# Performance work log

Measured on AMD Instinct MI355X. Metric: run time of the kernel, lower is better.

Reference implementation:

```python
import jax, jax.numpy as jnp
import numpy as np

N = 100000      # nodes
D = 64          # input feature dim
L0, L1 = 64, 32 # layer sizes
EP = 400000     # positive edges
EN = 400000     # negative edges
LAMB = 1.0


def _scatter_mean(feats, rows, num_nodes):
    # mean of feats grouped by destination node `rows`; empty nodes -> 0
    s = jax.ops.segment_sum(feats, rows, num_segments=num_nodes)
    c = jax.ops.segment_sum(jnp.ones((rows.shape[0],), feats.dtype), rows, num_segments=num_nodes)
    return s / jnp.maximum(c, 1.0)[:, None]


def _base_layer(x, edges, W, b):
    row, col = edges[0], edges[1]
    agg = _scatter_mean(x[col], row, x.shape[0])          # [N, D]
    return jnp.tanh(jnp.concatenate([agg, x], axis=1) @ W + b)


def _deep_layer(x1, x2, pos_edges, neg_edges, W, b):
    agg1 = _scatter_mean(x1[pos_edges[1]], pos_edges[0], x1.shape[0])
    agg2 = _scatter_mean(x2[neg_edges[1]], neg_edges[0], x2.shape[0])
    return jnp.tanh(jnp.concatenate([agg1, agg2, x1], axis=1) @ W + b)


def _xavier(key, shape):
    fan_in, fan_out = shape[0], shape[1]
    lim = np.sqrt(6.0 / (fan_in + fan_out)).astype(np.float32)
    return jax.random.uniform(key, shape, jnp.float32, -lim, lim)


def setup_inputs() -> dict:
    key = jax.random.key(0)
    ks = jax.random.split(key, 12)
    X = jax.random.normal(ks[0], (N, D), jnp.float32)
    W_pos0 = _xavier(ks[1], (2 * D, L0)); b_pos0 = jnp.zeros((L0,), jnp.float32)
    W_neg0 = _xavier(ks[2], (2 * D, L0)); b_neg0 = jnp.zeros((L0,), jnp.float32)
    W_pos1 = _xavier(ks[3], (3 * L0, L1)); b_pos1 = jnp.zeros((L1,), jnp.float32)
    W_neg1 = _xavier(ks[4], (3 * L0, L1)); b_neg1 = jnp.zeros((L1,), jnp.float32)
    W_reg = _xavier(ks[5], (4 * L1, 2))
    positive_edges = jax.random.randint(ks[6], (2, EP), 0, N)
    negative_edges = jax.random.randint(ks[7], (2, EN), 0, N)
    target = jax.random.randint(ks[8], (EP + EN,), 0, 2)
    pos_samples = jax.random.randint(ks[9], (EP,), 0, N)
    neg_samples = jax.random.randint(ks[10], (EN,), 0, N)
    return {"X": X, "W_pos0": W_pos0, "b_pos0": b_pos0, "W_neg0": W_neg0,
            "b_neg0": b_neg0, "W_pos1": W_pos1, "b_pos1": b_pos1,
            "W_neg1": W_neg1, "b_neg1": b_neg1, "W_reg": W_reg,
            "positive_edges": positive_edges, "negative_edges": negative_edges,
            "target": target, "pos_samples": pos_samples, "neg_samples": neg_samples}


def _triplet_loss(z, edges, samples):
    zi = z[edges[0]]
    zj = z[edges[1]]
    zk = z[samples]
    norm_ij = jnp.sum((zi - zj) ** 2, axis=1)
    norm_ik = jnp.sum((zj - zk) ** 2, axis=1)
    return jnp.mean(jnp.maximum(norm_ij - norm_ik, 0.0)), zi, zj


def reference(X, W_pos0, b_pos0, W_neg0, b_neg0, W_pos1, b_pos1,
              W_neg1, b_neg1, W_reg, positive_edges, negative_edges,
              target, pos_samples, neg_samples):
    h_pos = _base_layer(X, positive_edges, W_pos0, b_pos0)
    h_neg = _base_layer(X, negative_edges, W_neg0, b_neg0)
    h_pos2 = _deep_layer(h_pos, h_neg, positive_edges, negative_edges, W_pos1, b_pos1)
    h_neg2 = _deep_layer(h_neg, h_pos, positive_edges, negative_edges, W_neg1, b_neg1)
    z = jnp.concatenate([h_pos2, h_neg2], axis=1)  # [N, 2*L1]

    loss_pos, pzi, pzj = _triplet_loss(z, positive_edges, pos_samples)
    loss_neg, nzi, nzj = _triplet_loss(z, negative_edges, neg_samples)

    feats = jnp.concatenate([
        jnp.concatenate([pzi, pzj], axis=1),
        jnp.concatenate([nzi, nzj], axis=1)], axis=0)       # [EP+EN, 4*L1]
    logp = jax.nn.log_softmax(feats @ W_reg, axis=1)
    regress = -jnp.mean(jnp.take_along_axis(logp, target[:, None], axis=1))
    loss = regress + LAMB * (loss_pos + loss_neg)
    return (loss, z)
```

## Files before the change

### kernel.cpp

```cpp
#include <hip/hip_runtime.h>
#include <cstdint>

#define N_NODES 100000
#define EP_N 400000
#define EN_N 400000
#define NODE_BLOCKS ((N_NODES + 63) / 64)
#define SCHUNK 512
#define SBLK ((N_NODES + SCHUNK - 1) / SCHUNK)

#define BSTR 264
#define DSTR 392

#define XB_BLKS ((((N_NODES + 1) * 16) + 255) / 256)
#define WP_BLKS 112
#define CNT_BLKS (((EP_N + EN_N) + 255) / 256)

#define ACC_OFF 0
#define I_CNTP 16
#define I_CNTN (I_CNTP + N_NODES)
#define I_CURP (I_CNTN + N_NODES)
#define I_CURN (I_CURP + N_NODES)
#define I_OFFP (I_CURN + N_NODES)
#define I_OFFN (I_OFFP + N_NODES + 1)
#define I_CSRP (((I_OFFN + N_NODES + 1) + 3) & ~3)
#define CSR_SZ (EP_N + 4 * N_NODES)
#define I_CSRN (I_CSRP + CSR_SZ)
#define I_PART (I_CSRN + CSR_SZ)
#define F_XB (((I_PART + 2 * SBLK) + 15) & ~15)
#define F_HB (F_XB + 32 * (N_NODES + 1))
#define F_PN (F_HB + 64 * (N_NODES + 1))
#define F_ZQ (F_PN + 8 * N_NODES)
#define F_WT (((F_ZQ + 16 * N_NODES) + 15) & ~15)

typedef __attribute__((ext_vector_type(8))) short sh8;
typedef __attribute__((ext_vector_type(4))) float f32x4;

__device__ inline float bf2f(unsigned short u) {
    return __uint_as_float((unsigned)u << 16);
}
__device__ inline unsigned short f2bf(float v) {
    unsigned u = __float_as_uint(v);
    return (unsigned short)((u + 0x7FFFu + ((u >> 16) & 1u)) >> 16);
}
__device__ inline float lo_bf(unsigned u) { return __uint_as_float(u << 16); }
__device__ inline float hi_bf(unsigned u) { return __uint_as_float(u & 0xFFFF0000u); }

__global__ void prep_kernel(const float* __restrict__ X, unsigned short* __restrict__ xb,
                            const float* __restrict__ W0p, const float* __restrict__ W0n,
                            const float* __restrict__ W1p, const float* __restrict__ W1n,
                            unsigned short* __restrict__ wt,
                            const int* __restrict__ pe, const int* __restrict__ ne,
                            int* cp, int* cn) {
    int b = blockIdx.x;
    if (b < XB_BLKS) {
        int i = b * 256 + threadIdx.x;
        if (i < (N_NODES + 1) * 16) {
            ushort4 o = {0, 0, 0, 0};
            if (i < N_NODES * 16) {
                float4 v = ((const float4*)X)[i];
                o.x = f2bf(v.x); o.y = f2bf(v.y); o.z = f2bf(v.z); o.w = f2bf(v.w);
            }
            ((ushort4*)xb)[i] = o;
        }
    } else if (b < XB_BLKS + WP_BLKS) {
        int i = (b - XB_BLKS) * 256 + threadIdx.x;
        if (i < 8192) {
            int n = i >> 7, k = i & 127;
            wt[i] = f2bf(W0p[k * 64 + n]);
        } else if (i < 16384) {
            int j = i - 8192; int n = j >> 7, k = j & 127;
            wt[i] = f2bf(W0n[k * 64 + n]);
        } else if (i < 22528) {
            int j = i - 16384; int n = j / 192, k = j - n * 192;
            wt[i] = f2bf(W1p[k * 32 + n]);
        } else if (i < 28672) {
            int j = i - 22528; int n = j / 192, k = j - n * 192;
            wt[i] = f2bf(W1n[k * 32 + n]);
        }
    } else {
        int i = (b - XB_BLKS - WP_BLKS) * 256 + threadIdx.x;
        if (i < EP_N) {
            atomicAdd(&cp[pe[i]], 1);
        } else if (i < EP_N + EN_N) {
            atomicAdd(&cn[ne[i - EP_N]], 1);
        }
    }
}

__global__ __launch_bounds__(512) void scan_p1(const int* __restrict__ cntP,
                                               const int* __restrict__ cntN,
                                               int* part) {
    int l = blockIdx.x < SBLK ? 0 : 1;
    int blk = blockIdx.x - l * SBLK;
    const int* cnt = l == 0 ? cntP : cntN;
    int idx = blk * SCHUNK + threadIdx.x;
    int v = idx < N_NODES ? (cnt[idx] + 3) & ~3 : 0;
    __shared__ int tmp[512];
    tmp[threadIdx.x] = v;
    __syncthreads();
    for (int d = 256; d > 0; d >>= 1) {
        if (threadIdx.x < d) tmp[threadIdx.x] += tmp[threadIdx.x + d];
        __syncthreads();
    }
    if (threadIdx.x == 0) part[l * SBLK + blk] = tmp[0];
}

__global__ __launch_bounds__(512) void scan_p2(int* part) {
    int t = threadIdx.x;
    int l = t >> 8, idx = t & 255;
    int v = idx < SBLK ? part[l * SBLK + idx] : 0;
    __shared__ int tmp[512];
    int sb = l << 8;
    tmp[sb + idx] = v;
    __syncthreads();
    for (int d = 1; d < 256; d <<= 1) {
        int x = (idx >= d) ? tmp[sb + idx - d] : 0;
        __syncthreads();
        tmp[sb + idx] += x;
        __syncthreads();
    }
    if (idx < SBLK) part[l * SBLK + idx] = tmp[sb + idx] - v;
}

__global__ __launch_bounds__(512) void scan_p3(const int* __restrict__ cntP,
                                               const int* __restrict__ cntN,
                                               const int* __restrict__ part,
                                               int* offP, int* offN,
                                               int* csrP, int* csrN) {
    int l = blockIdx.x < SBLK ? 0 : 1;
    int blk = blockIdx.x - l * SBLK;
    const int* cnt = l == 0 ? cntP : cntN;
    int* off = l == 0 ? offP : offN;
    int* csr = l == 0 ? csrP : csrN;
    int base = part[l * SBLK + blk];
    int t = threadIdx.x;
    int gidx = blk * SCHUNK + t;
    int c = gidx < N_NODES ? cnt[gidx] : 0;
    int cpad = (c + 3) & ~3;
    __shared__ int tmp[512];
    tmp[t] = cpad;
    __syncthreads();
    for (int d = 1; d < 512; d <<= 1) {
        int x = (t >= d) ? tmp[t - d] : 0;
        __syncthreads();
        tmp[t] += x;
        __syncthreads();
    }
    int incl = tmp[t];
    if (gidx < N_NODES) {
        int o = base + incl - cpad;
        off[gidx] = o;
        for (int p = c; p < cpad; ++p) csr[o + p] = N_NODES;
    }
    if (gidx == N_NODES - 1) off[N_NODES] = base + incl;
}

__global__ void fill_kernel(const int* __restrict__ pe, const int* __restrict__ ne,
                            const int* __restrict__ offP, const int* __restrict__ offN,
                            int* curP, int* curN, int* csrP, int* csrN) {
    int e = blockIdx.x * 256 + threadIdx.x;
    if (e < EP_N) {
        int row = pe[e], col = pe[EP_N + e];
        int slot = atomicAdd(&curP[row], 1);
        csrP[offP[row] + slot] = col;
    } else if (e < EP_N + EN_N) {
        int e2 = e - EP_N;
        int row = ne[e2], col = ne[EN_N + e2];
        int slot = atomicAdd(&curN[row], 1);
        csrN[offN[row] + slot] = col;
    }
}

__device__ inline float gather_mean_b(const unsigned short* __restrict__ src,
                                      const int* __restrict__ csr,
                                      int st, int en, int cnt, int lane) {
    float s0 = 0.f, s1 = 0.f, s2 = 0.f, s3 = 0.f;
    for (int p = st; p < en; p += 4) {
        int4 c4 = *(const int4*)(csr + p);
        s0 += bf2f(src[c4.x * 64 + lane]);
        s1 += bf2f(src[c4.y * 64 + lane]);
        s2 += bf2f(src[c4.z * 64 + lane]);
        s3 += bf2f(src[c4.w * 64 + lane]);
    }
    return ((s0 + s1) + (s2 + s3)) / fmaxf((float)cnt, 1.0f);
}

__device__ inline void gather2(const unsigned* __restrict__ hb32,
                               const int* __restrict__ csr,
                               int st, int en, int cnt, int lane,
                               float& mp, float& mn) {
    float p0 = 0.f, p1 = 0.f, p2 = 0.f, p3 = 0.f;
    float n0 = 0.f, n1 = 0.f, n2 = 0.f, n3 = 0.f;
    for (int p = st; p < en; p += 4) {
        int4 c4 = *(const int4*)(csr + p);
        unsigned v0 = hb32[c4.x * 64 + lane];
        unsigned v1 = hb32[c4.y * 64 + lane];
        unsigned v2 = hb32[c4.z * 64 + lane];
        unsigned v3 = hb32[c4.w * 64 + lane];
        p0 += lo_bf(v0); n0 += hi_bf(v0);
        p1 += lo_bf(v1); n1 += hi_bf(v1);
        p2 += lo_bf(v2); n2 += hi_bf(v2);
        p3 += lo_bf(v3); n3 += hi_bf(v3);
    }
    float d = 1.0f / fmaxf((float)cnt, 1.0f);
    mp = ((p0 + p1) + (p2 + p3)) * d;
    mn = ((n0 + n1) + (n2 + n3)) * d;
}

__global__ __launch_bounds__(512) void base_both(
    const unsigned short* __restrict__ xb,
    const int* __restrict__ offP, const int* __restrict__ csrP,
    const int* __restrict__ offN, const int* __restrict__ csrN,
    const int* __restrict__ cntP, const int* __restrict__ cntN,
    const unsigned short* __restrict__ wt0,
    const float* __restrict__ bp0, const float* __restrict__ bn0,
    unsigned short* __restrict__ hboth) {
    __shared__ unsigned short lds[64 * BSTR];
    int tid = threadIdx.x, lane = tid & 63, w = tid >> 6;
    int base = blockIdx.x * 64;
    if (blockIdx.x == 0 && tid < 64) ((unsigned*)hboth)[N_NODES * 64 + tid] = 0u;
    for (int r = w * 8; r < w * 8 + 8; ++r) {
        int node = base + r;
        float gP = 0.f, gN = 0.f;
        unsigned short sx = 0;
        if (node < N_NODES) {
            gP = gather_mean_b(xb, csrP, offP[node], offP[node + 1], cntP[node], lane);
            gN = gather_mean_b(xb, csrN, offN[node], offN[node + 1], cntN[node], lane);
            sx = xb[node * 64 + lane];
        }
        unsigned short* rp = &lds[r * BSTR];
        rp[lane] = f2bf(gP);
        rp[64 + lane] = sx;
        rp[128 + lane] = f2bf(gN);
        rp[192 + lane] = sx;
    }
    __syncthreads();
    int wu = __builtin_amdgcn_readfirstlane(w);
    int mt = wu >> 1, half = wu & 1;
    int l15 = lane & 15, kq = lane >> 4;
    const unsigned short* wbase = wt0 + half * 8192;
    f32x4 acc[4];
#pragma unroll
    for (int nt = 0; nt < 4; ++nt) acc[nt] = (f32x4){0.f, 0.f, 0.f, 0.f};
    const unsigned short* arow = &lds[(mt * 16 + l15) * BSTR + half * 128 + kq * 8];
#pragma unroll
    for (int ks = 0; ks < 4; ++ks) {
        sh8 a = *(const sh8*)(arow + ks * 32);
#pragma unroll
        for (int nt = 0; nt < 4; ++nt) {
            sh8 bf = *(const sh8*)(wbase + (nt * 16 + l15) * 128 + ks * 32 + kq * 8);
            acc[nt] = __builtin_amdgcn_mfma_f32_16x16x32_bf16(a, bf, acc[nt], 0, 0, 0);
        }
    }
    __syncthreads();
    float* ht = (float*)lds;
    const float* bias = half ? bn0 : bp0;
#pragma unroll
    for (int nt = 0; nt < 4; ++nt) {
        int col = nt * 16 + l15;
        float bb = bias[col];
#pragma unroll
        for (int r = 0; r < 4; ++r) {
            int row = mt * 16 + kq * 4 + r;
            ht[row * 130 + half * 64 + col] = tanhf(acc[nt][r] + bb);
        }
    }
    __syncthreads();
    unsigned* hb32 = (unsigned*)hboth;
    for (int i = tid; i < 64 * 64; i += 512) {
        int rr = i >> 6, c = i & 63;
        int node = base + rr;
        if (node < N_NODES) {
            unsigned lo = f2bf(ht[rr * 130 + c]);
            unsigned hi = f2bf(ht[rr * 130 + 64 + c]);
            hb32[node * 64 + c] = lo | (hi << 16);
        }
    }
}

__global__ __launch_bounds__(512) void deep_both(
    const unsigned short* __restrict__ hb,
    const int* __restrict__ offP, const int* __restrict__ csrP,
    const int* __restrict__ offN, const int* __restrict__ csrN,
    const int* __restrict__ cntP, const int* __restrict__ cntN,
    const unsigned short* __restrict__ wt1,
    const float* __restrict__ bp1, const float* __restrict__ bn1,
    const float* __restrict__ Wreg, float* __restrict__ z,
    unsigned char* __restrict__ zq, float* __restrict__ pn) {
    __shared__ unsigned short lds[64 * DSTR];
    int tid = threadIdx.x, lane = tid & 63, w = tid >> 6;
    int base = blockIdx.x * 64;
    const unsigned* hb32 = (const unsigned*)hb;
    for (int r = w * 8; r < w * 8 + 8; ++r) {
        int node = base + r;
        float gPp = 0.f, gPn = 0.f, gNp = 0.f, gNn = 0.f, sp = 0.f, sn = 0.f;
        if (node < N_NODES) {
            gather2(hb32, csrP, offP[node], offP[node + 1], cntP[node], lane, gPp, gPn);
            gather2(hb32, csrN, offN[node], offN[node + 1], cntN[node], lane, gNp, gNn);
            unsigned self = hb32[node * 64 + lane];
            sp = lo_bf(self);
            sn = hi_bf(self);
        }
        unsigned short* rp = &lds[r * DSTR];
        rp[lane] = f2bf(gPp);
        rp[64 + lane] = f2bf(gNn);
        rp[128 + lane] = f2bf(sp);
        rp[192 + lane] = f2bf(gPn);
        rp[256 + lane] = f2bf(gNp);
        rp[320 + lane] = f2bf(sn);
    }
    __syncthreads();
    int wu = __builtin_amdgcn_readfirstlane(w);
    int mt = wu >> 1, half = wu & 1;
    int l15 = lane & 15, kq = lane >> 4;
    const unsigned short* wbase = wt1 + half * 6144;
    f32x4 acc[2];
    acc[0] = (f32x4){0.f, 0.f, 0.f, 0.f};
    acc[1] = (f32x4){0.f, 0.f, 0.f, 0.f};
    const unsigned short* arow = &lds[(mt * 16 + l15) * DSTR + half * 192 + kq * 8];
#pragma unroll
    for (int ks = 0; ks < 6; ++ks) {
        sh8 a = *(const sh8*)(arow + ks * 32);
#pragma unroll
        for (int nt = 0; nt < 2; ++nt) {
            sh8 bf = *(const sh8*)(wbase + (nt * 16 + l15) * 192 + ks * 32 + kq * 8);
            acc[nt] = __builtin_amdgcn_mfma_f32_16x16x32_bf16(a, bf, acc[nt], 0, 0, 0);
        }
    }
    __syncthreads();
    float* ot = (float*)lds;
    const float* bias = half ? bn1 : bp1;
#pragma unroll
    for (int nt = 0; nt < 2; ++nt) {
        int col = nt * 16 + l15;
        float bb = bias[col];
#pragma unroll
        for (int r = 0; r < 4; ++r) {
            int row = mt * 16 + kq * 4 + r;
            ot[row * 65 + half * 32 + col] = tanhf(acc[nt][r] + bb);
        }
    }
    __syncthreads();
    for (int r = w * 8; r < w * 8 + 8; ++r) {
        int node = base + r;
        if (node >= N_NODES) break;
        float v = ot[r * 65 + lane];
        z[node * 64 + lane] = v;
        int pq = __builtin_amdgcn_cvt_pk_fp8_f32(v, v, 0, false);
        zq[node * 64 + lane] = (unsigned char)(pq & 0xFF);
        float vq = __builtin_amdgcn_cvt_f32_fp8(pq, 0);
        float u0 = vq * Wreg[lane * 2 + 0];
        float u1 = vq * Wreg[lane * 2 + 1];
        float v0 = vq * Wreg[128 + lane * 2 + 0];
        float v1 = vq * Wreg[128 + lane * 2 + 1];
        float s = vq * vq;
#pragma unroll
        for (int off = 32; off; off >>= 1) {
            u0 += __shfl_xor(u0, off);
            u1 += __shfl_xor(u1, off);
            v0 += __shfl_xor(v0, off);
            v1 += __shfl_xor(v1, off);
            s += __shfl_xor(s, off);
        }
        if (lane == 0) {
            float4 st = {u0, u1, v0, v1};
            *(float4*)(pn + node * 8) = st;
            pn[node * 8 + 4] = s;
        }
    }
}

__global__ __launch_bounds__(256) void loss4_kernel(
    const unsigned char* __restrict__ zq, const float* __restrict__ pn,
    const int* __restrict__ pe, const int* __restrict__ ne,
    const int* __restrict__ ps, const int* __restrict__ ns,
    const int* __restrict__ tgt, float* acc) {
    int tid = threadIdx.x;
    int lane = tid & 63;
    int g = lane >> 4, sub = lane & 15;
    int wid = (blockIdx.x * 256 + tid) >> 6;
    int nw = (gridDim.x * 256) >> 6;
    float s_p = 0.f, s_n = 0.f, s_r = 0.f;
    const float q = 0.0625f;
    for (int eb = wid * 8; eb < EP_N + EN_N; eb += nw * 8) {
        int eA = eb + g, eB = eb + 4 + g;
        bool vA = eA < EP_N + EN_N, vB = eB < EP_N + EN_N;
        bool pA = eA < EP_N, pB = eB < EP_N;
        int iA = 0, jA = 0, kA = 0, tA = 0, iB = 0, jB = 0, kB = 0, tB = 0;
        if (vA) {
            if (pA) { iA = pe[eA]; jA = pe[EP_N + eA]; kA = ps[eA]; }
            else { int e2 = eA - EP_N; iA = ne[e2]; jA = ne[EN_N + e2]; kA = ns[e2]; }
            tA = tgt[eA];
        }
        if (vB) {
            if (pB) { iB = pe[eB]; jB = pe[EP_N + eB]; kB = ps[eB]; }
            else { int e2 = eB - EP_N; iB = ne[e2]; jB = ne[EN_N + e2]; kB = ns[e2]; }
            tB = tgt[eB];
        }
        unsigned ziA = *(const unsigned*)(zq + ((long long)iA << 6) + (sub << 2));
        unsigned zjA = *(const unsigned*)(zq + ((long long)jA << 6) + (sub << 2));
        unsigned zkA = *(const unsigned*)(zq + ((long long)kA << 6) + (sub << 2));
        unsigned ziB = *(const unsigned*)(zq + ((long long)iB << 6) + (sub << 2));
        unsigned zjB = *(const unsigned*)(zq + ((long long)jB << 6) + (sub << 2));
        unsigned zkB = *(const unsigned*)(zq + ((long long)kB << 6) + (sub << 2));
        const float* pniA = pn + ((long long)iA << 3);
        const float* pnjA = pn + ((long long)jA << 3);
        float u0A = pniA[0], u1A = pniA[1], siA = pniA[4];
        float v0A = pnjA[2], v1A = pnjA[3], sjA = pnjA[4];
        float skA = pn[((long long)kA << 3) + 4];
        const float* pniB = pn + ((long long)iB << 3);
        const float* pnjB = pn + ((long long)jB << 3);
        float u0B = pniB[0], u1B = pniB[1], siB = pniB[4];
        float v0B = pnjB[2], v1B = pnjB[3], sjB = pnjB[4];
        float skB = pn[((long long)kB << 3) + 4];
        float d1A, d2A, d1B, d2B;
        {
            float i0 = __builtin_amdgcn_cvt_f32_fp8(ziA, 0), i1 = __builtin_amdgcn_cvt_f32_fp8(ziA, 1);
            float i2 = __builtin_amdgcn_cvt_f32_fp8(ziA, 2), i3 = __builtin_amdgcn_cvt_f32_fp8(ziA, 3);
            float j0 = __builtin_amdgcn_cvt_f32_fp8(zjA, 0), j1 = __builtin_amdgcn_cvt_f32_fp8(zjA, 1);
            float j2 = __builtin_amdgcn_cvt_f32_fp8(zjA, 2), j3 = __builtin_amdgcn_cvt_f32_fp8(zjA, 3);
            float k0 = __builtin_amdgcn_cvt_f32_fp8(zkA, 0), k1 = __builtin_amdgcn_cvt_f32_fp8(zkA, 1);
            float k2 = __builtin_amdgcn_cvt_f32_fp8(zkA, 2), k3 = __builtin_amdgcn_cvt_f32_fp8(zkA, 3);
            d1A = fmaf(i0, j0, fmaf(i1, j1, fmaf(i2, j2, i3 * j3)));
            d2A = fmaf(j0, k0, fmaf(j1, k1, fmaf(j2, k2, j3 * k3)));
        }
        {
            float i0 = __builtin_amdgcn_cvt_f32_fp8(ziB, 0), i1 = __builtin_amdgcn_cvt_f32_fp8(ziB, 1);
            float i2 = __builtin_amdgcn_cvt_f32_fp8(ziB, 2), i3 = __builtin_amdgcn_cvt_f32_fp8(ziB, 3);
            float j0 = __builtin_amdgcn_cvt_f32_fp8(zjB, 0), j1 = __builtin_amdgcn_cvt_f32_fp8(zjB, 1);
            float j2 = __builtin_amdgcn_cvt_f32_fp8(zjB, 2), j3 = __builtin_amdgcn_cvt_f32_fp8(zjB, 3);
            float k0 = __builtin_amdgcn_cvt_f32_fp8(zkB, 0), k1 = __builtin_amdgcn_cvt_f32_fp8(zkB, 1);
            float k2 = __builtin_amdgcn_cvt_f32_fp8(zkB, 2), k3 = __builtin_amdgcn_cvt_f32_fp8(zkB, 3);
            d1B = fmaf(i0, j0, fmaf(i1, j1, fmaf(i2, j2, i3 * j3)));
            d2B = fmaf(j0, k0, fmaf(j1, k1, fmaf(j2, k2, j3 * k3)));
        }
#pragma unroll
        for (int off = 1; off < 16; off <<= 1) {
            d1A += __shfl_xor(d1A, off);
            d2A += __shfl_xor(d2A, off);
            d1B += __shfl_xor(d1B, off);
            d2B += __shfl_xor(d2B, off);
        }
        if (vA) {
            float nij = siA + sjA - 2.f * d1A;
            float nik = sjA + skA - 2.f * d2A;
            float tri = fmaxf(nij - nik, 0.f);
            float l0 = u0A + v0A, l1 = u1A + v1A;
            float m = fmaxf(l0, l1);
            float lse = m + logf(expf(l0 - m) + expf(l1 - m));
            s_r += (lse - (tA ? l1 : l0)) * q;
            if (pA) s_p += tri * q; else s_n += tri * q;
        }
        if (vB) {
            float nij = siB + sjB - 2.f * d1B;
            float nik = sjB + skB - 2.f * d2B;
            float tri = fmaxf(nij - nik, 0.f);
            float l0 = u0B + v0B, l1 = u1B + v1B;
            float m = fmaxf(l0, l1);
            float lse = m + logf(expf(l0 - m) + expf(l1 - m));
            s_r += (lse - (tB ? l1 : l0)) * q;
            if (pB) s_p += tri * q; else s_n += tri * q;
        }
    }
#pragma unroll
    for (int off = 32; off; off >>= 1) {
        s_p += __shfl_xor(s_p, off);
        s_n += __shfl_xor(s_n, off);
        s_r += __shfl_xor(s_r, off);
    }
    __shared__ float red[3][4];
    int w = tid >> 6;
    if (lane == 0) {
        red[0][w] = s_p; red[1][w] = s_n; red[2][w] = s_r;
    }
    __syncthreads();
    if (tid == 0) {
        atomicAdd(&acc[0], red[0][0] + red[0][1] + red[0][2] + red[0][3]);
        atomicAdd(&acc[1], red[1][0] + red[1][1] + red[1][2] + red[1][3]);
        atomicAdd(&acc[2], red[2][0] + red[2][1] + red[2][2] + red[2][3]);
    }
}

__global__ void finalize_kernel(const float* __restrict__ acc, float* out) {
    out[0] = acc[2] / (float)(EP_N + EN_N) +
             1.0f * (acc[0] / (float)EP_N + acc[1] / (float)EN_N);
}

extern "C" void kernel_launch(void* const* d_in, const int* in_sizes, int n_in,
                              void* d_out, int out_size, void* d_ws, size_t ws_size,
                              hipStream_t stream) {
    const float* X = (const float*)d_in[0];
    const float* W_pos0 = (const float*)d_in[1];
    const float* b_pos0 = (const float*)d_in[2];
    const float* W_neg0 = (const float*)d_in[3];
    const float* b_neg0 = (const float*)d_in[4];
    const float* W_pos1 = (const float*)d_in[5];
    const float* b_pos1 = (const float*)d_in[6];
    const float* W_neg1 = (const float*)d_in[7];
    const float* b_neg1 = (const float*)d_in[8];
    const float* W_reg = (const float*)d_in[9];
    const int* pe = (const int*)d_in[10];
    const int* ne = (const int*)d_in[11];
    const int* target = (const int*)d_in[12];
    const int* ps = (const int*)d_in[13];
    const int* ns = (const int*)d_in[14];
    float* out = (float*)d_out;
    float* ws = (float*)d_ws;
    int* wsi = (int*)d_ws;

    float* acc = ws + ACC_OFF;
    int* cntP = wsi + I_CNTP;
    int* cntN = wsi + I_CNTN;
    int* curP = wsi + I_CURP;
    int* curN = wsi + I_CURN;
    int* offP = wsi + I_OFFP;
    int* offN = wsi + I_OFFN;
    int* csrP = wsi + I_CSRP;
    int* csrN = wsi + I_CSRN;
    int* part = wsi + I_PART;
    unsigned short* xb = (unsigned short*)(ws + F_XB);
    unsigned short* hboth = (unsigned short*)(ws + F_HB);
    float* pn = ws + F_PN;
    unsigned char* zq = (unsigned char*)(ws + F_ZQ);
    unsigned short* wt = (unsigned short*)(ws + F_WT);
    float* z = out + 1;

    hipMemsetAsync(ws, 0, (size_t)(16 + 4 * N_NODES) * sizeof(float), stream);

    prep_kernel<<<XB_BLKS + WP_BLKS + CNT_BLKS, 256, 0, stream>>>(
        X, xb, W_pos0, W_neg0, W_pos1, W_neg1, wt, pe, ne, cntP, cntN);
    scan_p1<<<2 * SBLK, 512, 0, stream>>>(cntP, cntN, part);
    scan_p2<<<1, 512, 0, stream>>>(part);
    scan_p3<<<2 * SBLK, 512, 0, stream>>>(cntP, cntN, part, offP, offN, csrP, csrN);
    fill_kernel<<<(EP_N + EN_N + 255) / 256, 256, 0, stream>>>(pe, ne, offP, offN,
                                                               curP, curN, csrP, csrN);

    base_both<<<NODE_BLOCKS, 512, 0, stream>>>(xb, offP, csrP, offN, csrN, cntP, cntN,
                                               wt, b_pos0, b_neg0, hboth);
    deep_both<<<NODE_BLOCKS, 512, 0, stream>>>(hboth, offP, csrP, offN, csrN, cntP, cntN,
                                               wt + 16384, b_pos1, b_neg1,
                                               W_reg, z, zq, pn);

    loss4_kernel<<<2048, 256, 0, stream>>>(zq, pn, pe, ne, ps, ns, target, acc);
    finalize_kernel<<<1, 1, 0, stream>>>(acc, out);
}
```

Before: 410.4 us.

## Interleave pos/neg CSR gathers and pack per-edge indices and node stats

The base and deep layers now walk the positive and negative neighbour lists in one interleaved loop, so twice as many independent gather loads are in flight per iteration. The prep kernel packs each edge's (i, j, sample, target) into an int4 array. The per-node stats are split into two float4 arrays (u0,u1,s) and (v0,v1,s), so the loss kernel does one vector load for the indices and one per node instead of many scalar loads. The cost is an extra pass that writes 12.8 MB of packed indices, plus higher register pressure in the gather loops.

```diff
diff --git a/kernel.cpp b/kernel.cpp
--- a/kernel.cpp
+++ b/kernel.cpp
@@ -14,6 +14,7 @@
 #define XB_BLKS ((((N_NODES + 1) * 16) + 255) / 256)
 #define WP_BLKS 112
 #define CNT_BLKS (((EP_N + EN_N) + 255) / 256)
+#define EI_BLKS CNT_BLKS
 
 #define ACC_OFF 0
 #define I_CNTP 16
@@ -26,10 +27,12 @@
 #define CSR_SZ (EP_N + 4 * N_NODES)
 #define I_CSRN (I_CSRP + CSR_SZ)
 #define I_PART (I_CSRN + CSR_SZ)
-#define F_XB (((I_PART + 2 * SBLK) + 15) & ~15)
+#define I_EIDX (((I_PART + 2 * SBLK) + 3) & ~3)
+#define F_XB (((I_EIDX + 4 * (EP_N + EN_N)) + 15) & ~15)
 #define F_HB (F_XB + 32 * (N_NODES + 1))
-#define F_PN (F_HB + 64 * (N_NODES + 1))
-#define F_ZQ (F_PN + 8 * N_NODES)
+#define F_PNU (F_HB + 64 * (N_NODES + 1))
+#define F_PNV (F_PNU + 4 * N_NODES)
+#define F_ZQ (F_PNV + 4 * N_NODES)
 #define F_WT (((F_ZQ + 16 * N_NODES) + 15) & ~15)
 
 typedef __attribute__((ext_vector_type(8))) short sh8;
@@ -50,7 +53,9 @@
                             const float* __restrict__ W1p, const float* __restrict__ W1n,
                             unsigned short* __restrict__ wt,
                             const int* __restrict__ pe, const int* __restrict__ ne,
-                            int* cp, int* cn) {
+                            const int* __restrict__ ps, const int* __restrict__ ns,
+                            const int* __restrict__ tgt,
+                            int* cp, int* cn, int4* __restrict__ eidx) {
     int b = blockIdx.x;
     if (b < XB_BLKS) {
         int i = b * 256 + threadIdx.x;
@@ -77,12 +82,22 @@
             int j = i - 22528; int n = j / 192, k = j - n * 192;
             wt[i] = f2bf(W1n[k * 32 + n]);
         }
-    } else {
+    } else if (b < XB_BLKS + WP_BLKS + CNT_BLKS) {
         int i = (b - XB_BLKS - WP_BLKS) * 256 + threadIdx.x;
         if (i < EP_N) {
             atomicAdd(&cp[pe[i]], 1);
         } else if (i < EP_N + EN_N) {
             atomicAdd(&cn[ne[i - EP_N]], 1);
+        }
+    } else {
+        int e = (b - XB_BLKS - WP_BLKS - CNT_BLKS) * 256 + threadIdx.x;
+        if (e < EP_N) {
+            int4 q = {pe[e], pe[EP_N + e], ps[e], tgt[e]};
+            eidx[e] = q;
+        } else if (e < EP_N + EN_N) {
+            int e2 = e - EP_N;
+            int4 q = {ne[e2], ne[EN_N + e2], ns[e2], tgt[e]};
+            eidx[e] = q;
         }
     }
 }
@@ -171,40 +186,100 @@
     }
 }
 
-__device__ inline float gather_mean_b(const unsigned short* __restrict__ src,
-                                      const int* __restrict__ csr,
-                                      int st, int en, int cnt, int lane) {
-    float s0 = 0.f, s1 = 0.f, s2 = 0.f, s3 = 0.f;
-    for (int p = st; p < en; p += 4) {
-        int4 c4 = *(const int4*)(csr + p);
-        s0 += bf2f(src[c4.x * 64 + lane]);
-        s1 += bf2f(src[c4.y * 64 + lane]);
-        s2 += bf2f(src[c4.z * 64 + lane]);
-        s3 += bf2f(src[c4.w * 64 + lane]);
-    }
-    return ((s0 + s1) + (s2 + s3)) / fmaxf((float)cnt, 1.0f);
-}
-
-__device__ inline void gather2(const unsigned* __restrict__ hb32,
-                               const int* __restrict__ csr,
-                               int st, int en, int cnt, int lane,
-                               float& mp, float& mn) {
-    float p0 = 0.f, p1 = 0.f, p2 = 0.f, p3 = 0.f;
-    float n0 = 0.f, n1 = 0.f, n2 = 0.f, n3 = 0.f;
-    for (int p = st; p < en; p += 4) {
-        int4 c4 = *(const int4*)(csr + p);
-        unsigned v0 = hb32[c4.x * 64 + lane];
-        unsigned v1 = hb32[c4.y * 64 + lane];
-        unsigned v2 = hb32[c4.z * 64 + lane];
-        unsigned v3 = hb32[c4.w * 64 + lane];
-        p0 += lo_bf(v0); n0 += hi_bf(v0);
-        p1 += lo_bf(v1); n1 += hi_bf(v1);
-        p2 += lo_bf(v2); n2 += hi_bf(v2);
-        p3 += lo_bf(v3); n3 += hi_bf(v3);
-    }
-    float d = 1.0f / fmaxf((float)cnt, 1.0f);
-    mp = ((p0 + p1) + (p2 + p3)) * d;
-    mn = ((n0 + n1) + (n2 + n3)) * d;
+__device__ inline void gmb2(const unsigned short* __restrict__ src,
+                            const int* __restrict__ csrP, int pP, int enP, int cP,
+                            const int* __restrict__ csrN, int pN, int enN, int cN,
+                            int lane, float& mP, float& mN) {
+    float a0 = 0.f, a1 = 0.f, a2 = 0.f, a3 = 0.f;
+    float b0 = 0.f, b1 = 0.f, b2 = 0.f, b3 = 0.f;
+    while (pP < enP && pN < enN) {
+        int4 ca = *(const int4*)(csrP + pP);
+        int4 cb = *(const int4*)(csrN + pN);
+        a0 += bf2f(src[ca.x * 64 + lane]);
+        a1 += bf2f(src[ca.y * 64 + lane]);
+        a2 += bf2f(src[ca.z * 64 + lane]);
+        a3 += bf2f(src[ca.w * 64 + lane]);
+        b0 += bf2f(src[cb.x * 64 + lane]);
+        b1 += bf2f(src[cb.y * 64 + lane]);
+        b2 += bf2f(src[cb.z * 64 + lane]);
+        b3 += bf2f(src[cb.w * 64 + lane]);
+        pP += 4; pN += 4;
+    }
+    for (; pP < enP; pP += 4) {
+        int4 ca = *(const int4*)(csrP + pP);
+        a0 += bf2f(src[ca.x * 64 + lane]);
+        a1 += bf2f(src[ca.y * 64 + lane]);
+        a2 += bf2f(src[ca.z * 64 + lane]);
+        a3 += bf2f(src[ca.w * 64 + lane]);
+    }
+    for (; pN < enN; pN += 4) {
+        int4 cb = *(const int4*)(csrN + pN);
+        b0 += bf2f(src[cb.x * 64 + lane]);
+        b1 += bf2f(src[cb.y * 64 + lane]);
+        b2 += bf2f(src[cb.z * 64 + lane]);
+        b3 += bf2f(src[cb.w * 64 + lane]);
+    }
+    mP = ((a0 + a1) + (a2 + a3)) / fmaxf((float)cP, 1.f);
+    mN = ((b0 + b1) + (b2 + b3)) / fmaxf((float)cN, 1.f);
+}
+
+__device__ inline void gd2(const unsigned* __restrict__ hb32,
+                           const int* __restrict__ csrP, int pP, int enP, int cP,
+                           const int* __restrict__ csrN, int pN, int enN, int cN,
+                           int lane,
+                           float& gPp, float& gPn, float& gNp, float& gNn) {
+    float ap0 = 0.f, ap1 = 0.f, ap2 = 0.f, ap3 = 0.f;
+    float an0 = 0.f, an1 = 0.f, an2 = 0.f, an3 = 0.f;
+    float bp0 = 0.f, bp1 = 0.f, bp2 = 0.f, bp3 = 0.f;
+    float bn0 = 0.f, bn1 = 0.f, bn2 = 0.f, bn3 = 0.f;
+    while (pP < enP && pN < enN) {
+        int4 ca = *(const int4*)(csrP + pP);
+        int4 cb = *(const int4*)(csrN + pN);
+        unsigned va0 = hb32[ca.x * 64 + lane];
+        unsigned va1 = hb32[ca.y * 64 + lane];
+        unsigned va2 = hb32[ca.z * 64 + lane];
+        unsigned va3 = hb32[ca.w * 64 + lane];
+        unsigned vb0 = hb32[cb.x * 64 + lane];
+        unsigned vb1 = hb32[cb.y * 64 + lane];
+        unsigned vb2 = hb32[cb.z * 64 + lane];
+        unsigned vb3 = hb32[cb.w * 64 + lane];
+        ap0 += lo_bf(va0); an0 += hi_bf(va0);
+        ap1 += lo_bf(va1); an1 += hi_bf(va1);
+        ap2 += lo_bf(va2); an2 += hi_bf(va2);
+        ap3 += lo_bf(va3); an3 += hi_bf(va3);
+        bp0 += lo_bf(vb0); bn0 += hi_bf(vb0);
+        bp1 += lo_bf(vb1); bn1 += hi_bf(vb1);
+        bp2 += lo_bf(vb2); bn2 += hi_bf(vb2);
+        bp3 += lo_bf(vb3); bn3 += hi_bf(vb3);
+        pP += 4; pN += 4;
+    }
+    for (; pP < enP; pP += 4) {
+        int4 ca = *(const int4*)(csrP + pP);
+        unsigned va0 = hb32[ca.x * 64 + lane];
+        unsigned va1 = hb32[ca.y * 64 + lane];
+        unsigned va2 = hb32[ca.z * 64 + lane];
+        unsigned va3 = hb32[ca.w * 64 + lane];
+        ap0 += lo_bf(va0); an0 += hi_bf(va0);
+        ap1 += lo_bf(va1); an1 += hi_bf(va1);
+        ap2 += lo_bf(va2); an2 += hi_bf(va2);
+        ap3 += lo_bf(va3); an3 += hi_bf(va3);
+    }
+    for (; pN < enN; pN += 4) {
+        int4 cb = *(const int4*)(csrN + pN);
+        unsigned vb0 = hb32[cb.x * 64 + lane];
+        unsigned vb1 = hb32[cb.y * 64 + lane];
+        unsigned vb2 = hb32[cb.z * 64 + lane];
+        unsigned vb3 = hb32[cb.w * 64 + lane];
+        bp0 += lo_bf(vb0); bn0 += hi_bf(vb0);
+        bp1 += lo_bf(vb1); bn1 += hi_bf(vb1);
+        bp2 += lo_bf(vb2); bn2 += hi_bf(vb2);
+        bp3 += lo_bf(vb3); bn3 += hi_bf(vb3);
+    }
+    float rP = 1.f / fmaxf((float)cP, 1.f), rN = 1.f / fmaxf((float)cN, 1.f);
+    gPp = ((ap0 + ap1) + (ap2 + ap3)) * rP;
+    gPn = ((an0 + an1) + (an2 + an3)) * rP;
+    gNp = ((bp0 + bp1) + (bp2 + bp3)) * rN;
+    gNn = ((bn0 + bn1) + (bn2 + bn3)) * rN;
 }
 
 __global__ __launch_bounds__(512) void base_both(
@@ -224,8 +299,8 @@
         float gP = 0.f, gN = 0.f;
         unsigned short sx = 0;
         if (node < N_NODES) {
-            gP = gather_mean_b(xb, csrP, offP[node], offP[node + 1], cntP[node], lane);
-            gN = gather_mean_b(xb, csrN, offN[node], offN[node + 1], cntN[node], lane);
+            gmb2(xb, csrP, offP[node], offP[node + 1], cntP[node],
+                 csrN, offN[node], offN[node + 1], cntN[node], lane, gP, gN);
             sx = xb[node * 64 + lane];
         }
         unsigned short* rp = &lds[r * BSTR];
@@ -286,7 +361,8 @@
     const unsigned short* __restrict__ wt1,
     const float* __restrict__ bp1, const float* __restrict__ bn1,
     const float* __restrict__ Wreg, float* __restrict__ z,
-    unsigned char* __restrict__ zq, float* __restrict__ pn) {
+    unsigned char* __restrict__ zq, float4* __restrict__ pnu,
+    float4* __restrict__ pnv) {
     __shared__ unsigned short lds[64 * DSTR];
     int tid = threadIdx.x, lane = tid & 63, w = tid >> 6;
     int base = blockIdx.x * 64;
@@ -295,8 +371,9 @@
         int node = base + r;
         float gPp = 0.f, gPn = 0.f, gNp = 0.f, gNn = 0.f, sp = 0.f, sn = 0.f;
         if (node < N_NODES) {
-            gather2(hb32, csrP, offP[node], offP[node + 1], cntP[node], lane, gPp, gPn);
-            gather2(hb32, csrN, offN[node], offN[node + 1], cntN[node], lane, gNp, gNn);
+            gd2(hb32, csrP, offP[node], offP[node + 1], cntP[node],
+                csrN, offN[node], offN[node + 1], cntN[node], lane,
+                gPp, gPn, gNp, gNn);
             unsigned self = hb32[node * 64 + lane];
             sp = lo_bf(self);
             sn = hi_bf(self);
@@ -363,18 +440,17 @@
             s += __shfl_xor(s, off);
         }
         if (lane == 0) {
-            float4 st = {u0, u1, v0, v1};
-            *(float4*)(pn + node * 8) = st;
-            pn[node * 8 + 4] = s;
-        }
-    }
-}
-
-__global__ __launch_bounds__(256) void loss4_kernel(
-    const unsigned char* __restrict__ zq, const float* __restrict__ pn,
-    const int* __restrict__ pe, const int* __restrict__ ne,
-    const int* __restrict__ ps, const int* __restrict__ ns,
-    const int* __restrict__ tgt, float* acc) {
+            float4 su = {u0, u1, s, 0.f};
+            float4 sv = {v0, v1, s, 0.f};
+            pnu[node] = su;
+            pnv[node] = sv;
+        }
+    }
+}
+
+__global__ __launch_bounds__(256) void loss5_kernel(
+    const unsigned char* __restrict__ zq, const float4* __restrict__ pnu,
+    const float4* __restrict__ pnv, const int4* __restrict__ eidx, float* acc) {
     int tid = threadIdx.x;
     int lane = tid & 63;
     int g = lane >> 4, sub = lane & 15;
@@ -386,33 +462,20 @@
         int eA = eb + g, eB = eb + 4 + g;
         bool vA = eA < EP_N + EN_N, vB = eB < EP_N + EN_N;
         bool pA = eA < EP_N, pB = eB < EP_N;
-        int iA = 0, jA = 0, kA = 0, tA = 0, iB = 0, jB = 0, kB = 0, tB = 0;
-        if (vA) {
-            if (pA) { iA = pe[eA]; jA = pe[EP_N + eA]; kA = ps[eA]; }
-            else { int e2 = eA - EP_N; iA = ne[e2]; jA = ne[EN_N + e2]; kA = ns[e2]; }
-            tA = tgt[eA];
-        }
-        if (vB) {
-            if (pB) { iB = pe[eB]; jB = pe[EP_N + eB]; kB = ps[eB]; }
-            else { int e2 = eB - EP_N; iB = ne[e2]; jB = ne[EN_N + e2]; kB = ns[e2]; }
-            tB = tgt[eB];
-        }
-        unsigned ziA = *(const unsigned*)(zq + ((long long)iA << 6) + (sub << 2));
-        unsigned zjA = *(const unsigned*)(zq + ((long long)jA << 6) + (sub << 2));
-        unsigned zkA = *(const unsigned*)(zq + ((long long)kA << 6) + (sub << 2));
-        unsigned ziB = *(const unsigned*)(zq + ((long long)iB << 6) + (sub << 2));
-        unsigned zjB = *(const unsigned*)(zq + ((long long)jB << 6) + (sub << 2));
-        unsigned zkB = *(const unsigned*)(zq + ((long long)kB << 6) + (sub << 2));
-        const float* pniA = pn + ((long long)iA << 3);
-        const float* pnjA = pn + ((long long)jA << 3);
-        float u0A = pniA[0], u1A = pniA[1], siA = pniA[4];
-        float v0A = pnjA[2], v1A = pnjA[3], sjA = pnjA[4];
-        float skA = pn[((long long)kA << 3) + 4];
-        const float* pniB = pn + ((long long)iB << 3);
-        const float* pnjB = pn + ((long long)jB << 3);
-        float u0B = pniB[0], u1B = pniB[1], siB = pniB[4];
-        float v0B = pnjB[2], v1B = pnjB[3], sjB = pnjB[4];
-        float skB = pn[((long long)kB << 3) + 4];
+        int4 qA = eidx[vA ? eA : 0];
+        int4 qB = eidx[vB ? eB : 0];
+        unsigned ziA = *(const unsigned*)(zq + ((long long)qA.x << 6) + (sub << 2));
+        unsigned zjA = *(const unsigned*)(zq + ((long long)qA.y << 6) + (sub << 2));
+        unsigned zkA = *(const unsigned*)(zq + ((long long)qA.z << 6) + (sub << 2));
+        unsigned ziB = *(const unsigned*)(zq + ((long long)qB.x << 6) + (sub << 2));
+        unsigned zjB = *(const unsigned*)(zq + ((long long)qB.y << 6) + (sub << 2));
+        unsigned zkB = *(const unsigned*)(zq + ((long long)qB.z << 6) + (sub << 2));
+        float4 uA = pnu[qA.x];
+        float4 wA = pnv[qA.y];
+        float skA = pnu[qA.z].z;
+        float4 uB = pnu[qB.x];
+        float4 wB = pnv[qB.y];
+        float skB = pnu[qB.z].z;
         float d1A, d2A, d1B, d2B;
         {
             float i0 = __builtin_amdgcn_cvt_f32_fp8(ziA, 0), i1 = __builtin_amdgcn_cvt_f32_fp8(ziA, 1);
@@ -442,23 +505,23 @@
             d2B += __shfl_xor(d2B, off);
         }
         if (vA) {
-            float nij = siA + sjA - 2.f * d1A;
-            float nik = sjA + skA - 2.f * d2A;
+            float nij = uA.z + wA.z - 2.f * d1A;
+            float nik = wA.z + skA - 2.f * d2A;
             float tri = fmaxf(nij - nik, 0.f);
-            float l0 = u0A + v0A, l1 = u1A + v1A;
+            float l0 = uA.x + wA.x, l1 = uA.y + wA.y;
             float m = fmaxf(l0, l1);
             float lse = m + logf(expf(l0 - m) + expf(l1 - m));
-            s_r += (lse - (tA ? l1 : l0)) * q;
+            s_r += (lse - (qA.w ? l1 : l0)) * q;
             if (pA) s_p += tri * q; else s_n += tri * q;
         }
         if (vB) {
-            float nij = siB + sjB - 2.f * d1B;
-            float nik = sjB + skB - 2.f * d2B;
+            float nij = uB.z + wB.z - 2.f * d1B;
+            float nik = wB.z + skB - 2.f * d2B;
             float tri = fmaxf(nij - nik, 0.f);
-            float l0 = u0B + v0B, l1 = u1B + v1B;
+            float l0 = uB.x + wB.x, l1 = uB.y + wB.y;
             float m = fmaxf(l0, l1);
             float lse = m + logf(expf(l0 - m) + expf(l1 - m));
-            s_r += (lse - (tB ? l1 : l0)) * q;
+            s_r += (lse - (qB.w ? l1 : l0)) * q;
             if (pB) s_p += tri * q; else s_n += tri * q;
         }
     }
@@ -518,17 +581,20 @@
     int* csrP = wsi + I_CSRP;
     int* csrN = wsi + I_CSRN;
     int* part = wsi + I_PART;
+    int4* eidx = (int4*)(wsi + I_EIDX);
     unsigned short* xb = (unsigned short*)(ws + F_XB);
     unsigned short* hboth = (unsigned short*)(ws + F_HB);
-    float* pn = ws + F_PN;
+    float4* pnu = (float4*)(ws + F_PNU);
+    float4* pnv = (float4*)(ws + F_PNV);
     unsigned char* zq = (unsigned char*)(ws + F_ZQ);
     unsigned short* wt = (unsigned short*)(ws + F_WT);
     float* z = out + 1;
 
     hipMemsetAsync(ws, 0, (size_t)(16 + 4 * N_NODES) * sizeof(float), stream);
 
-    prep_kernel<<<XB_BLKS + WP_BLKS + CNT_BLKS, 256, 0, stream>>>(
-        X, xb, W_pos0, W_neg0, W_pos1, W_neg1, wt, pe, ne, cntP, cntN);
+    prep_kernel<<<XB_BLKS + WP_BLKS + CNT_BLKS + EI_BLKS, 256, 0, stream>>>(
+        X, xb, W_pos0, W_neg0, W_pos1, W_neg1, wt, pe, ne, ps, ns, target,
+        cntP, cntN, eidx);
     scan_p1<<<2 * SBLK, 512, 0, stream>>>(cntP, cntN, part);
     scan_p2<<<1, 512, 0, stream>>>(part);
     scan_p3<<<2 * SBLK, 512, 0, stream>>>(cntP, cntN, part, offP, offN, csrP, csrN);
@@ -539,8 +605,8 @@
                                                wt, b_pos0, b_neg0, hboth);
     deep_both<<<NODE_BLOCKS, 512, 0, stream>>>(hboth, offP, csrP, offN, csrN, cntP, cntN,
                                                wt + 16384, b_pos1, b_neg1,
-                                               W_reg, z, zq, pn);
-
-    loss4_kernel<<<2048, 256, 0, stream>>>(zq, pn, pe, ne, ps, ns, target, acc);
+                                               W_reg, z, zq, pnu, pnv);
+
+    loss5_kernel<<<2048, 256, 0, stream>>>(zq, pnu, pnv, eidx, acc);
     finalize_kernel<<<1, 1, 0, stream>>>(acc, out);
 }
```

New measurement: 379.9 us. 7.4% less time.
